# Kernel tuning notes

Measured on AMD Instinct MI355X. Metric: run time of the kernel, lower is better.

## Reference

```python
import jax, jax.numpy as jnp
import numpy as np


def conv(x, w, b=None, stride=1, pad=0):
    out = jax.lax.conv_general_dilated(x, w, (stride, stride), [(pad, pad), (pad, pad)],
                                       dimension_numbers=('NCHW', 'OIHW', 'NCHW'))
    if b is not None:
        out = out + b[None, :, None, None]
    return out


def fsm(x, att_w, conv_w):
    # FeatureSelectionModule: global-avg-pool -> 1x1 conv -> sigmoid gate, residual, 1x1 proj
    gap = jnp.mean(x, axis=(2, 3), keepdims=True)
    atten = jax.nn.sigmoid(conv(gap, att_w))
    return conv(x + x * atten, conv_w)


def mdcn(x, offset, mask, weight, bias, pad=1, G=8):
    # Modulated deformable conv v2: stride 1, dilation 1, conv groups 1, G deformable groups.
    N, C, H, W = x.shape
    Co, Ci, kh, kw = weight.shape
    K = kh * kw
    Cg = C // G
    off = offset.reshape(N, G, 2, K, H, W)          # per-group (y, x) offsets per kernel tap
    msk = mask.reshape(N, G, 1, K, H, W)
    ky, kx = jnp.meshgrid(jnp.arange(kh), jnp.arange(kw), indexing='ij')
    py = (jnp.arange(H, dtype=x.dtype)[None, None, None, :, None] - pad) + ky.reshape(1, 1, K, 1, 1) + off[:, :, 0]
    px = (jnp.arange(W, dtype=x.dtype)[None, None, None, None, :] - pad) + kx.reshape(1, 1, K, 1, 1) + off[:, :, 1]
    y0 = jnp.floor(py)
    x0 = jnp.floor(px)
    wy1 = py - y0
    wy0 = 1.0 - wy1
    wx1 = px - x0
    wx0 = 1.0 - wx1
    xg = x.reshape(N, G, Cg, H * W)

    def gather(iy, ix):
        valid = (iy >= 0) & (iy <= H - 1) & (ix >= 0) & (ix <= W - 1)
        idx = (jnp.clip(iy, 0, H - 1) * W + jnp.clip(ix, 0, W - 1)).astype(jnp.int32)
        v = jnp.take_along_axis(xg, idx.reshape(N, G, 1, K * H * W), axis=3)
        return v.reshape(N, G, Cg, K, H, W) * valid[:, :, None].astype(x.dtype)

    val = ((wy0 * wx0)[:, :, None] * gather(y0, x0)
         + (wy0 * wx1)[:, :, None] * gather(y0, x0 + 1)
         + (wy1 * wx0)[:, :, None] * gather(y0 + 1, x0)
         + (wy1 * wx1)[:, :, None] * gather(y0 + 1, x0 + 1))
    val = val * msk                                   # [N,G,Cg,K,H,W]
    out = jnp.einsum('ngckhw,ogck->nohw', val, weight.reshape(Co, G, Cg, K))
    return out + bias[None, :, None, None]


def align(feat_l, feat_s, att_w, fsm_w, off_w, om_w, om_b, dcn_w, dcn_b):
    # FeatureAlign_V2
    N, Cs, H, W = feat_s.shape[0], feat_s.shape[1], feat_l.shape[2], feat_l.shape[3]
    feat_up = jax.image.resize(feat_s, (N, Cs, H, W), 'bilinear')  # align_corners=False
    feat_arm = fsm(feat_l, att_w, fsm_w)
    off_feat = conv(jnp.concatenate([feat_arm, feat_up * 2.0], axis=1), off_w)
    om = conv(off_feat, om_w, om_b, pad=1)            # conv_offset_mask: 3*G*K channels
    o1, o2, mk = jnp.split(om, 3, axis=1)
    offset = jnp.concatenate([o1, o2], axis=1)
    mask = jax.nn.sigmoid(mk)
    feat_align = jax.nn.relu(mdcn(feat_up, offset, mask, dcn_w, dcn_b))
    return feat_align + feat_arm


def setup_inputs() -> dict:
    key = jax.random.key(0)
    ks = iter(jax.random.split(key, 64))

    def w(shape):
        fan_in = shape[1] * shape[2] * shape[3]
        return jax.random.normal(next(ks), shape, jnp.float32) / np.float32(np.sqrt(fan_in))

    def b(n):
        return jnp.zeros((n,), jnp.float32)

    d = {}
    d['c2'] = jax.random.normal(next(ks), (1, 256, 128, 128), jnp.float32)
    d['c3'] = jax.random.normal(next(ks), (1, 512, 64, 64), jnp.float32)
    d['c4'] = jax.random.normal(next(ks), (1, 1024, 32, 32), jnp.float32)
    d['c5'] = jax.random.normal(next(ks), (1, 2048, 16, 16), jnp.float32)
    OC = 256
    OM = 8 * 3 * 9  # deformable_groups * (2 offsets + 1 mask) * k*k = 216
    for tag, in_nc in (('16', 1024), ('8', 512), ('4', 256)):
        d['att_w' + tag] = w((in_nc, in_nc, 1, 1))
        d['fsm_w' + tag] = w((OC, in_nc, 1, 1))
        d['off_w' + tag] = w((OC, 2 * OC, 1, 1))
        d['om_w' + tag] = w((OM, OC, 3, 3))
        d['om_b' + tag] = b(OM)
        d['dcn_w' + tag] = w((OC, OC, 3, 3))
        d['dcn_b' + tag] = b(OC)
        d['out_w' + tag] = w((OC, OC, 3, 3))
        d['out_b' + tag] = b(OC)
    d['lat_w'] = w((OC, 2048, 1, 1))
    d['lat_b'] = b(OC)
    return d


def reference(c2, c3, c4, c5,
              att_w16, fsm_w16, off_w16, om_w16, om_b16, dcn_w16, dcn_b16, out_w16, out_b16,
              att_w8, fsm_w8, off_w8, om_w8, om_b8, dcn_w8, dcn_b8, out_w8, out_b8,
              att_w4, fsm_w4, off_w4, om_w4, om_b4, dcn_w4, dcn_b4, out_w4, out_b4,
              lat_w, lat_b):
    # top-down pass, coarsest first (matches FAN.forward with reversed inputs)
    p5 = conv(c5, lat_w, lat_b)
    f16 = align(c4, p5, att_w16, fsm_w16, off_w16, om_w16, om_b16, dcn_w16, dcn_b16)
    p4 = conv(f16, out_w16, out_b16, pad=1)
    f8 = align(c3, f16, att_w8, fsm_w8, off_w8, om_w8, om_b8, dcn_w8, dcn_b8)
    p3 = conv(f8, out_w8, out_b8, pad=1)
    f4 = align(c2, f8, att_w4, fsm_w4, off_w4, om_w4, om_b4, dcn_w4, dcn_b4)
    p2 = conv(f4, out_w4, out_b4, pad=1)
    return (p2, p3, p4, p5)
```

## Files before the change

kernel.cpp:

```cpp
#include <hip/hip_runtime.h>
#include <hip/hip_bf16.h>

typedef __hip_bfloat16 bf16;
typedef __attribute__((ext_vector_type(8))) short bf16x8;
typedef __attribute__((ext_vector_type(4))) float floatx4;

__device__ __forceinline__ float b2f(bf16 v) { return __bfloat162float(v); }
__device__ __forceinline__ bf16 f2b(float v) { return __float2bfloat16(v); }
__device__ __forceinline__ float us2f(unsigned short u) {
  union { unsigned int i; float f; } v; v.i = ((unsigned int)u) << 16; return v.f;
}
__device__ __forceinline__ unsigned short f2us(float f) {
  bf16 h = f2b(f); return *(unsigned short*)&h;
}

__global__ __launch_bounds__(256) void gap_kernel(const float* __restrict__ x,
                                                  float* __restrict__ gap,
                                                  int HW, float inv) {
  int c = blockIdx.x;
  const float* p = x + (size_t)c * HW;
  float s = 0.f;
  for (int i = threadIdx.x; i < HW; i += 256) s += p[i];
  __shared__ float red[256];
  red[threadIdx.x] = s;
  __syncthreads();
  for (int w = 128; w > 0; w >>= 1) {
    if (threadIdx.x < w) red[threadIdx.x] += red[threadIdx.x + w];
    __syncthreads();
  }
  if (threadIdx.x == 0) gap[c] = red[0] * inv;
}

__global__ __launch_bounds__(256) void atten_kernel(const float* __restrict__ w,
                                                    const float* __restrict__ gap,
                                                    float* __restrict__ scale, int Ci) {
  int wave = threadIdx.x >> 6, lane = threadIdx.x & 63;
  int o = blockIdx.x * 4 + wave;
  const float4* wr = (const float4*)(w + (size_t)o * Ci);
  const float4* g4 = (const float4*)gap;
  int n4 = Ci >> 2;
  float s = 0.f;
  for (int i = lane; i < n4; i += 64) {
    float4 a = wr[i], b = g4[i];
    s += a.x * b.x + a.y * b.y + a.z * b.z + a.w * b.w;
  }
#pragma unroll
  for (int off = 32; off > 0; off >>= 1) s += __shfl_down(s, off);
  if (lane == 0) scale[o] = 1.f + 1.f / (1.f + expf(-s));
}

__global__ __launch_bounds__(256) void upsample2x_nhwc_kernel(
    const bf16* __restrict__ src, bf16* __restrict__ dst, int Hs, int Ws) {
  int p = blockIdx.x;
  int c = threadIdx.x;
  int W = Ws * 2;
  int y = p / W, x = p - y * W;
  float fy = y * 0.5f - 0.25f;
  float fx = x * 0.5f - 0.25f;
  int y0 = (int)floorf(fy), x0 = (int)floorf(fx);
  float wy1 = fy - (float)y0, wx1 = fx - (float)x0;
  int y0c = min(max(y0, 0), Hs - 1);
  int y1c = min(max(y0 + 1, 0), Hs - 1);
  int x0c = min(max(x0, 0), Ws - 1);
  int x1c = min(max(x0 + 1, 0), Ws - 1);
  float v00 = b2f(src[(size_t)(y0c * Ws + x0c) * 256 + c]);
  float v01 = b2f(src[(size_t)(y0c * Ws + x1c) * 256 + c]);
  float v10 = b2f(src[(size_t)(y1c * Ws + x0c) * 256 + c]);
  float v11 = b2f(src[(size_t)(y1c * Ws + x1c) * 256 + c]);
  float v = (1.f - wy1) * ((1.f - wx1) * v00 + wx1 * v01)
          + wy1 * ((1.f - wx1) * v10 + wx1 * v11);
  dst[(size_t)p * 256 + c] = f2b(v);
}

__global__ __launch_bounds__(256) void packw1_kernel(const float* __restrict__ w,
                                                     bf16* __restrict__ BP, int K) {
  int idx = blockIdx.x * 256 + threadIdx.x;
  int j = idx & 7;
  int o = (idx >> 3) & 255;
  int kc8 = idx >> 11;
  int k = kc8 * 8 + j;
  BP[idx] = f2b(w[(size_t)o * K + k]);
}

__global__ __launch_bounds__(256) void packwd_kernel(const float* __restrict__ w,
                                                     bf16* __restrict__ BP) {
  int idx = blockIdx.x * 256 + threadIdx.x;
  int j = idx & 7;
  int o = (idx >> 3) & 255;
  int k8 = idx >> 11;
  int k = k8 * 8 + j;
  int tap = k >> 8;
  int ci = k & 255;
  BP[idx] = f2b(w[((size_t)o * 256 + ci) * 9 + tap]);
}

__global__ __launch_bounds__(256) void packw3_kernel(const float* __restrict__ w,
                                                     bf16* __restrict__ BP,
                                                     int Ci, int Co) {
  int idx = blockIdx.x * 256 + threadIdx.x;
  int total = Ci * 9 * 256;
  if (idx >= total) return;
  int j = idx & 7;
  int t1 = idx >> 3;
  int o = t1 & 255;
  int t2 = t1 >> 8;
  int q = t2 & 3;
  int t3 = t2 >> 2;
  int tap = t3 % 9;
  int c = t3 / 9;
  int ci = c * 32 + q * 8 + j;
  float v = (o < Co) ? w[((size_t)o * Ci + ci) * 9 + tap] : 0.f;
  BP[idx] = f2b(v);
}

template <bool NCHW1, typename TA1>
__global__ __launch_bounds__(256) void conv1x1_mfma_kernel(
    const TA1* __restrict__ A1, const float* __restrict__ scaleA,
    const bf16* __restrict__ A2, float scaleB,
    int Ci1, int Ci2, int HW,
    const bf16* __restrict__ BP, const float* __restrict__ bias,
    float* __restrict__ out1, bf16* __restrict__ out2, int ns2) {
  __shared__ __align__(16) bf16 sA[1024];
  int p0 = blockIdx.x * 32;
  int tid = threadIdx.x;
  int pix = tid & 31, sub = tid >> 5;
  int pix2 = tid >> 3, sub8 = tid & 7;
  int lane = tid & 63, wave = tid >> 6;
  int pg = wave & 1, cg = wave >> 1;
  int q = lane >> 4, n = lane & 15;

  floatx4 acc[4];
#pragma unroll
  for (int nt = 0; nt < 4; ++nt) acc[nt] = (floatx4)0.f;

  int nch = (Ci1 + Ci2) >> 5;
  for (int kc = 0; kc < nch; ++kc) {
    int ci0 = kc << 5;
    if (NCHW1 && ci0 < Ci1) {
#pragma unroll
      for (int it = 0; it < 4; ++it) {
        int cil = it * 8 + sub;
        float x = (float)A1[(size_t)(ci0 + cil) * HW + p0 + pix];
        if (scaleA) x *= scaleA[ci0 + cil];
        sA[((cil >> 3) * 32 + pix) * 8 + (cil & 7)] = f2b(x);
      }
    } else {
      const bf16* src; int cb; bool scl;
      if (!NCHW1 && ci0 < Ci1) {
        src = (const bf16*)(const void*)A1; cb = ci0; scl = false;
      } else {
        src = A2; cb = ci0 - Ci1; scl = true;
      }
      ushort4 raw = *(const ushort4*)&src[(size_t)(p0 + pix2) * 256 + cb + sub8 * 4];
      if (scl) {
        raw.x = f2us(us2f(raw.x) * scaleB);
        raw.y = f2us(us2f(raw.y) * scaleB);
        raw.z = f2us(us2f(raw.z) * scaleB);
        raw.w = f2us(us2f(raw.w) * scaleB);
      }
      *(ushort4*)&sA[((sub8 >> 1) * 32 + pix2) * 8 + (sub8 & 1) * 4] = raw;
    }
    __syncthreads();
    bf16x8 a = *(const bf16x8*)&sA[(q * 32 + pg * 16 + n) * 8];
    const bf16* bp = BP + ((size_t)(kc * 4 + q) * 256 + blockIdx.y * 128 + cg * 64) * 8;
#pragma unroll
    for (int nt = 0; nt < 4; ++nt) {
      bf16x8 b = *(const bf16x8*)&bp[(nt * 16 + n) * 8];
      acc[nt] = __builtin_amdgcn_mfma_f32_16x16x32_bf16(a, b, acc[nt], 0, 0, 0);
    }
    __syncthreads();
  }

  int pbase = p0 + pg * 16 + q * 4;
#pragma unroll
  for (int nt = 0; nt < 4; ++nt) {
    int o = blockIdx.y * 128 + cg * 64 + nt * 16 + n;
    float bv = bias ? bias[o] : 0.f;
#pragma unroll
    for (int r = 0; r < 4; ++r) {
      float v = acc[nt][r] + bv;
      if (out1) out1[(size_t)o * HW + pbase + r] = v;
      if (out2) out2[(size_t)(pbase + r) * ns2 + o] = f2b(v);
    }
  }
}

__global__ __launch_bounds__(256) void conv1x1_part_kernel(
    const float* __restrict__ A1, int HW,
    const bf16* __restrict__ BP, float* __restrict__ PART) {
  __shared__ __align__(16) bf16 sA[1024];
  int p0 = blockIdx.x * 32;
  int tid = threadIdx.x;
  int pix = tid & 31, sub = tid >> 5;
  int lane = tid & 63, wave = tid >> 6;
  int pg = wave & 1, cg = wave >> 1;
  int q = lane >> 4, n = lane & 15;

  floatx4 acc[4];
#pragma unroll
  for (int nt = 0; nt < 4; ++nt) acc[nt] = (floatx4)0.f;

  int kc0 = blockIdx.z * 8;
  for (int kcl = 0; kcl < 8; ++kcl) {
    int kc = kc0 + kcl;
    int ci0 = kc << 5;
#pragma unroll
    for (int it = 0; it < 4; ++it) {
      int cil = it * 8 + sub;
      sA[((cil >> 3) * 32 + pix) * 8 + (cil & 7)] =
          f2b(A1[(size_t)(ci0 + cil) * HW + p0 + pix]);
    }
    __syncthreads();
    bf16x8 a = *(const bf16x8*)&sA[(q * 32 + pg * 16 + n) * 8];
    const bf16* bp = BP + ((size_t)(kc * 4 + q) * 256 + blockIdx.y * 128 + cg * 64) * 8;
#pragma unroll
    for (int nt = 0; nt < 4; ++nt) {
      bf16x8 b = *(const bf16x8*)&bp[(nt * 16 + n) * 8];
      acc[nt] = __builtin_amdgcn_mfma_f32_16x16x32_bf16(a, b, acc[nt], 0, 0, 0);
    }
    __syncthreads();
  }

  int pbase = p0 + pg * 16 + q * 4;
#pragma unroll
  for (int nt = 0; nt < 4; ++nt) {
    int o = blockIdx.y * 128 + cg * 64 + nt * 16 + n;
#pragma unroll
    for (int r = 0; r < 4; ++r)
      PART[((size_t)blockIdx.z * 256 + o) * HW + pbase + r] = acc[nt][r];
  }
}

__global__ __launch_bounds__(256) void reduce_p5_kernel(
    const float* __restrict__ PART, const float* __restrict__ bias,
    float* __restrict__ out1, bf16* __restrict__ out2, int HW, int KS) {
  int o = blockIdx.x;
  int p = threadIdx.x;
  float s = bias[o];
  for (int z = 0; z < KS; ++z) s += PART[((size_t)z * 256 + o) * HW + p];
  out1[(size_t)o * HW + p] = s;
  out2[(size_t)p * 256 + o] = f2b(s);
}

template <int S>
__global__ __launch_bounds__(256) void conv3x3v2_kernel(
    const bf16* __restrict__ in, const bf16* __restrict__ BP,
    const float* __restrict__ bias,
    int H, int W, int Co,
    float* __restrict__ out1, bf16* __restrict__ out2, int ns2) {
  constexpr int P = 32 * S + 2;
  constexpr int TASKS = 3 * P * 8;
  constexpr int ITS = (TASKS + 255) / 256;
  __shared__ __align__(16) bf16 sA[2][4 * 3 * P * 8];
  int HW = H * W;
  int segs = W / (32 * S);
  int y = blockIdx.x / segs;
  int x0 = (blockIdx.x - y * segs) * (32 * S);
  int tid = threadIdx.x;
  int lane = tid & 63, wave = tid >> 6;
  int pg = wave & 1, cg = wave >> 1;
  int q = lane >> 4, n = lane & 15;

  int dstIdx[ITS], srcOff[ITS];
  bool act[ITS], val[ITS];
#pragma unroll
  for (int it = 0; it < ITS; ++it) {
    int tt = it * 256 + tid;
    act[it] = (tt < TASKS);
    int sub8 = tt & 7;
    int rp = tt >> 3;
    int row = rp / P;
    int pxl = rp - row * P;
    int yy = y + row - 1;
    int xg = x0 + pxl - 1;
    bool v = act[it] && ((unsigned)yy < (unsigned)H) && ((unsigned)xg < (unsigned)W);
    val[it] = v;
    srcOff[it] = v ? ((yy * W + xg) * 256 + sub8 * 4) : 0;
    dstIdx[it] = (((sub8 >> 1) * 3 + row) * P + pxl) * 8 + (sub8 & 1) * 4;
  }

  ushort4 pv[ITS];
  auto load_regs = [&](int kc) {
    int cb = kc << 5;
#pragma unroll
    for (int it = 0; it < ITS; ++it) {
      ushort4 z = {0, 0, 0, 0};
      pv[it] = val[it] ? *(const ushort4*)&in[(size_t)srcOff[it] + cb] : z;
    }
  };
  auto store_lds = [&](int buf) {
#pragma unroll
    for (int it = 0; it < ITS; ++it)
      if (act[it]) *(ushort4*)&sA[buf][dstIdx[it]] = pv[it];
  };

  floatx4 acc[S][4];
#pragma unroll
  for (int s = 0; s < S; ++s)
#pragma unroll
    for (int nt = 0; nt < 4; ++nt) acc[s][nt] = (floatx4)0.f;

  load_regs(0);
  store_lds(0);
  __syncthreads();
  load_regs(1);

  for (int kc = 0; kc < 8; ++kc) {
    const bf16* sv = &sA[kc & 1][0];
    const bf16* bpc = BP + (size_t)kc * 73728;
#pragma unroll
    for (int tap = 0; tap < 9; ++tap) {
      int ty = tap / 3, tx = tap % 3;
      bf16x8 a[S];
#pragma unroll
      for (int s = 0; s < S; ++s)
        a[s] = *(const bf16x8*)&sv[((q * 3 + ty) * P + tx + s * 32 + pg * 16 + n) * 8];
      const bf16* bp = bpc + ((size_t)(tap * 4 + q) * 256 + blockIdx.y * 128 + cg * 64) * 8;
#pragma unroll
      for (int nt = 0; nt < 4; ++nt) {
        bf16x8 b = *(const bf16x8*)&bp[(nt * 16 + n) * 8];
#pragma unroll
        for (int s = 0; s < S; ++s)
          acc[s][nt] = __builtin_amdgcn_mfma_f32_16x16x32_bf16(a[s], b, acc[s][nt], 0, 0, 0);
      }
    }
    if (kc < 7) {
      store_lds((kc + 1) & 1);
      __syncthreads();
      if (kc < 6) load_regs(kc + 2);
    }
  }

#pragma unroll
  for (int s = 0; s < S; ++s) {
    int pbase = y * W + x0 + s * 32 + pg * 16 + q * 4;
#pragma unroll
    for (int nt = 0; nt < 4; ++nt) {
      int o = blockIdx.y * 128 + cg * 64 + nt * 16 + n;
      if (o < Co) {
        float bv = bias ? bias[o] : 0.f;
#pragma unroll
        for (int r = 0; r < 4; ++r) {
          float v = acc[s][nt][r] + bv;
          if (out1) out1[(size_t)o * HW + pbase + r] = v;
          if (out2) out2[(size_t)(pbase + r) * ns2 + o] = f2b(v);
        }
      }
    }
  }
}

__global__ __launch_bounds__(512, 4) void mdcn_mfma_kernel(
    const bf16* __restrict__ UPn, const bf16* __restrict__ OM,
    const bf16* __restrict__ BP, const float* __restrict__ dcn_b,
    const bf16* __restrict__ ARM, bf16* __restrict__ F,
    int H, int W, int wshift) {
  __shared__ __align__(16) bf16 sval[2][32 * 272];
  __shared__ float4 mw[2304];
  __shared__ int mi[2304];
  int pb = blockIdx.x * 32;
  int tid = threadIdx.x;

  for (int t2 = tid; t2 < 2304; t2 += 512) {
    int px_ = t2 & 31, g = (t2 >> 5) & 7, tap = t2 >> 8;
    int ky = tap / 3, kx = tap - ky * 3;
    int p = pb + px_;
    int y = p >> wshift, x = p & (W - 1);
    const bf16* omp = OM + (size_t)p * 216;
    float dy = b2f(omp[g * 18 + tap]);
    float dx = b2f(omp[g * 18 + 9 + tap]);
    float mm = 1.f / (1.f + expf(-b2f(omp[144 + g * 9 + tap])));
    float fpy = (float)(y - 1 + ky) + dy;
    float fpx = (float)(x - 1 + kx) + dx;
    fpy = fminf(fmaxf(fpy, -1.0e4f), 1.0e4f);
    fpx = fminf(fmaxf(fpx, -1.0e4f), 1.0e4f);
    float fy0 = floorf(fpy), fx0 = floorf(fpx);
    float wy1 = fpy - fy0, wx1 = fpx - fx0;
    float wy0 = 1.f - wy1, wx0 = 1.f - wx1;
    int iy0 = (int)fy0, ix0 = (int)fx0;
    bool vy0 = (unsigned)iy0 < (unsigned)H;
    bool vy1 = (unsigned)(iy0 + 1) < (unsigned)H;
    bool vx0 = (unsigned)ix0 < (unsigned)W;
    bool vx1 = (unsigned)(ix0 + 1) < (unsigned)W;
    float w00 = (vy0 && vx0) ? mm * wy0 * wx0 : 0.f;
    float w01 = (vy0 && vx1) ? mm * wy0 * wx1 : 0.f;
    float w10 = (vy1 && vx0) ? mm * wy1 * wx0 : 0.f;
    float w11 = (vy1 && vx1) ? mm * wy1 * wx1 : 0.f;
    int iy0c = min(max(iy0, 0), H - 1);
    int iy1c = min(max(iy0 + 1, 0), H - 1);
    int ix0c = min(max(ix0, 0), W - 1);
    int ix1c = min(max(ix0 + 1, 0), W - 1);
    mw[t2] = make_float4(w00, w01, w10, w11);
    mi[t2] = (iy0c * W + ix0c) | ((ix1c - ix0c) << 20) | ((iy1c - iy0c) << 21);
  }
  __syncthreads();

  int px = tid >> 4, l2 = tid & 15;
  int lane = tid & 63, wave = tid >> 6;
  int q = lane >> 4, n = lane & 15;
  int rowb = l2 >> 2;
  int woff = px * 8 + (l2 & 3) * 2;

  floatx4 acc[2][2];
#pragma unroll
  for (int m = 0; m < 2; ++m)
#pragma unroll
    for (int nt = 0; nt < 2; ++nt) acc[m][nt] = (floatx4)0.f;

  auto gather = [&](int t) {
    bf16* sv = &sval[t & 1][0];
    int base = t * 256 + px;
#pragma unroll
    for (int g = 0; g < 8; ++g) {
      float4 wv = mw[base + g * 32];
      int mv = mi[base + g * 32];
      int idx = mv & 0x3FFFF;
      int dxs = (mv >> 20) & 1;
      int dyW = ((mv >> 21) & 1) * W;
      const bf16* up = UPn + (size_t)idx * 256 + g * 32 + l2 * 2;
      ushort2 u00 = *(const ushort2*)(up);
      ushort2 u01 = *(const ushort2*)(up + dxs * 256);
      ushort2 u10 = *(const ushort2*)(up + dyW * 256);
      ushort2 u11 = *(const ushort2*)(up + (dyW + dxs) * 256);
      float s0 = wv.x * us2f(u00.x) + wv.y * us2f(u01.x)
               + wv.z * us2f(u10.x) + wv.w * us2f(u11.x);
      float s1 = wv.x * us2f(u00.y) + wv.y * us2f(u01.y)
               + wv.z * us2f(u10.y) + wv.w * us2f(u11.y);
      ushort2 o2;
      o2.x = f2us(s0);
      o2.y = f2us(s1);
      *(ushort2*)&sv[(g * 4 + rowb) * 272 + woff] = o2;
    }
  };

  gather(0);
  for (int t = 0; t < 9; ++t) {
    __syncthreads();
    if (t < 8) gather(t + 1);
    const bf16* sv = &sval[t & 1][0];
    const bf16* bpt = BP + ((size_t)(t * 32) * 256 + wave * 32) * 8;
#pragma unroll
    for (int kc = 0; kc < 8; ++kc) {
      int R = kc * 4 + q;
      bf16x8 a0 = *(const bf16x8*)&sv[R * 272 + n * 8];
      bf16x8 a1 = *(const bf16x8*)&sv[R * 272 + (16 + n) * 8];
      const bf16* bp = bpt + (size_t)R * 2048;
      bf16x8 b0 = *(const bf16x8*)&bp[n * 8];
      bf16x8 b1 = *(const bf16x8*)&bp[(16 + n) * 8];
      acc[0][0] = __builtin_amdgcn_mfma_f32_16x16x32_bf16(a0, b0, acc[0][0], 0, 0, 0);
      acc[0][1] = __builtin_amdgcn_mfma_f32_16x16x32_bf16(a0, b1, acc[0][1], 0, 0, 0);
      acc[1][0] = __builtin_amdgcn_mfma_f32_16x16x32_bf16(a1, b0, acc[1][0], 0, 0, 0);
      acc[1][1] = __builtin_amdgcn_mfma_f32_16x16x32_bf16(a1, b1, acc[1][1], 0, 0, 0);
    }
  }

#pragma unroll
  for (int m = 0; m < 2; ++m) {
#pragma unroll
    for (int nt = 0; nt < 2; ++nt) {
      int o = wave * 32 + nt * 16 + n;
      float bv = dcn_b[o];
#pragma unroll
      for (int r = 0; r < 4; ++r) {
        int p = pb + m * 16 + q * 4 + r;
        float v = fmaxf(acc[m][nt][r] + bv, 0.f) + b2f(ARM[(size_t)p * 256 + o]);
        F[(size_t)p * 256 + o] = f2b(v);
      }
    }
  }
}

extern "C" void kernel_launch(void* const* d_in, const int* in_sizes, int n_in,
                              void* d_out, int out_size, void* d_ws, size_t ws_size,
                              hipStream_t stream) {
  const float* c2 = (const float*)d_in[0];
  const float* c3 = (const float*)d_in[1];
  const float* c4 = (const float*)d_in[2];
  const float* c5 = (const float*)d_in[3];
  const float* lat_w = (const float*)d_in[31];
  const float* lat_b = (const float*)d_in[32];
  float* out = (float*)d_out;
  (void)ws_size; (void)in_sizes; (void)n_in; (void)out_size;

  const size_t p2_off = 0;
  const size_t p3_off = 4194304;
  const size_t p4_off = p3_off + 1048576;
  const size_t p5_off = p4_off + 262144;

  char* ws = (char*)d_ws;
  bf16* UPn = (bf16*)(ws);
  bf16* ARM = (bf16*)(ws + 8388608);
  bf16* FB  = (bf16*)(ws + 16777216);
  bf16* P5N = (bf16*)(ws + 25165824);
  bf16* BPB = (bf16*)(ws + 25296896);
  float* GAP = (float*)(ws + 26476544);
  float* SC  = (float*)(ws + 26484736);
  bf16* OM = (bf16*)(out + p2_off);
  float* PART = (float*)ws;

  packw1_kernel<<<2048, 256, 0, stream>>>(lat_w, BPB, 2048);
  conv1x1_part_kernel<<<dim3(8, 2, 8), 256, 0, stream>>>(c5, 256, BPB, PART);
  reduce_p5_kernel<<<256, 256, 0, stream>>>(PART, lat_b, out + p5_off, P5N, 256, 8);

  struct Lv {
    const float* featl; int Ci; int H; int W; int wshift;
    float* pdst; int wbase;
  };
  Lv levels[3] = {
      {c4, 1024, 32, 32, 5, out + p4_off, 4},
      {c3, 512, 64, 64, 6, out + p3_off, 13},
      {c2, 256, 128, 128, 7, out + p2_off, 22},
  };

  for (int li = 0; li < 3; ++li) {
    const Lv& L = levels[li];
    const float* att_w = (const float*)d_in[L.wbase + 0];
    const float* fsm_w = (const float*)d_in[L.wbase + 1];
    const float* off_w = (const float*)d_in[L.wbase + 2];
    const float* om_w  = (const float*)d_in[L.wbase + 3];
    const float* om_b  = (const float*)d_in[L.wbase + 4];
    const float* dcn_w = (const float*)d_in[L.wbase + 5];
    const float* dcn_b = (const float*)d_in[L.wbase + 6];
    const float* out_w = (const float*)d_in[L.wbase + 7];
    const float* out_b = (const float*)d_in[L.wbase + 8];
    int HW = L.H * L.W;

    upsample2x_nhwc_kernel<<<HW, 256, 0, stream>>>(
        (li == 0) ? P5N : FB, UPn, L.H / 2, L.W / 2);
    gap_kernel<<<L.Ci, 256, 0, stream>>>(L.featl, GAP, HW, 1.f / (float)HW);
    atten_kernel<<<L.Ci / 4, 256, 0, stream>>>(att_w, GAP, SC, L.Ci);
    packw1_kernel<<<L.Ci, 256, 0, stream>>>(fsm_w, BPB, L.Ci);
    conv1x1_mfma_kernel<true, float><<<dim3(HW / 32, 2), 256, 0, stream>>>(
        L.featl, SC, nullptr, 0.f, L.Ci, 0, HW, BPB, nullptr,
        nullptr, ARM, 256);
    packw1_kernel<<<512, 256, 0, stream>>>(off_w, BPB, 512);
    conv1x1_mfma_kernel<false, bf16><<<dim3(HW / 32, 2), 256, 0, stream>>>(
        ARM, nullptr, UPn, 2.f, 256, 256, HW, BPB, nullptr,
        nullptr, FB, 256);
    packw3_kernel<<<2304, 256, 0, stream>>>(om_w, BPB, 256, 216);
    if (li == 2)
      conv3x3v2_kernel<2><<<dim3(HW / 64, 2), 256, 0, stream>>>(
          FB, BPB, om_b, L.H, L.W, 216, nullptr, OM, 216);
    else
      conv3x3v2_kernel<1><<<dim3(HW / 32, 2), 256, 0, stream>>>(
          FB, BPB, om_b, L.H, L.W, 216, nullptr, OM, 216);
    packwd_kernel<<<2304, 256, 0, stream>>>(dcn_w, BPB);
    mdcn_mfma_kernel<<<HW / 32, 512, 0, stream>>>(
        UPn, OM, BPB, dcn_b, ARM, FB, L.H, L.W, L.wshift);
    packw3_kernel<<<2304, 256, 0, stream>>>(out_w, BPB, 256, 256);
    if (li == 2)
      conv3x3v2_kernel<2><<<dim3(HW / 64, 2), 256, 0, stream>>>(
          FB, BPB, out_b, L.H, L.W, 256, L.pdst, nullptr, 256);
    else
      conv3x3v2_kernel<1><<<dim3(HW / 32, 2), 256, 0, stream>>>(
          FB, BPB, out_b, L.H, L.W, 256, L.pdst, nullptr, 256);
  }
}
```

Measured before the change: 733.3 us.

## Restructure deformable conv kernel: 64-pixel tiles, per-thread sampling, vectorized gathers

The MDCN kernel now covers 64 pixels per block instead of 32, so each weight fragment loaded from global memory feeds four M-tiles of MFMA instead of two. The shared-memory precompute table of bilinear weights and indices is gone. Each thread computes its own sample coordinates per tap inside the gather, and loads 8-channel vectors (four 16-byte loads per corner) instead of 2-channel pairs. This cuts weight traffic and shared-memory bookkeeping per pixel, but adds recomputation of offsets, higher register pressure (occupancy hint lowered to 2) and half as many blocks.

```diff
diff --git a/kernel.cpp b/kernel.cpp
--- a/kernel.cpp
+++ b/kernel.cpp
@@ -4,6 +4,7 @@
 typedef __hip_bfloat16 bf16;
 typedef __attribute__((ext_vector_type(8))) short bf16x8;
 typedef __attribute__((ext_vector_type(4))) float floatx4;
+typedef __attribute__((ext_vector_type(8))) unsigned short ushort8v;
 
 __device__ __forceinline__ float b2f(bf16 v) { return __bfloat162float(v); }
 __device__ __forceinline__ bf16 f2b(float v) { return __float2bfloat16(v); }
@@ -350,26 +351,35 @@
   }
 }
 
-__global__ __launch_bounds__(512, 4) void mdcn_mfma_kernel(
+__global__ __launch_bounds__(512, 2) void mdcn_mfma_kernel(
     const bf16* __restrict__ UPn, const bf16* __restrict__ OM,
     const bf16* __restrict__ BP, const float* __restrict__ dcn_b,
     const bf16* __restrict__ ARM, bf16* __restrict__ F,
     int H, int W, int wshift) {
-  __shared__ __align__(16) bf16 sval[2][32 * 272];
-  __shared__ float4 mw[2304];
-  __shared__ int mi[2304];
-  int pb = blockIdx.x * 32;
+  __shared__ __align__(16) bf16 sval[2][32 * 520];
+  int pb = blockIdx.x * 64;
   int tid = threadIdx.x;
-
-  for (int t2 = tid; t2 < 2304; t2 += 512) {
-    int px_ = t2 & 31, g = (t2 >> 5) & 7, tap = t2 >> 8;
-    int ky = tap / 3, kx = tap - ky * 3;
-    int p = pb + px_;
-    int y = p >> wshift, x = p & (W - 1);
-    const bf16* omp = OM + (size_t)p * 216;
-    float dy = b2f(omp[g * 18 + tap]);
-    float dx = b2f(omp[g * 18 + 9 + tap]);
-    float mm = 1.f / (1.f + expf(-b2f(omp[144 + g * 9 + tap])));
+  int g = tid >> 6;
+  int px = tid & 63;
+  int p = pb + px;
+  int y = p >> wshift, x = p & (W - 1);
+  const bf16* omp = OM + (size_t)p * 216 + g * 18;
+  const bf16* omm = OM + (size_t)p * 216 + 144 + g * 9;
+  int lane = tid & 63, wave = tid >> 6;
+  int q = lane >> 4, n = lane & 15;
+
+  floatx4 acc[4][2];
+#pragma unroll
+  for (int m = 0; m < 4; ++m)
+#pragma unroll
+    for (int nt = 0; nt < 2; ++nt) acc[m][nt] = (floatx4)0.f;
+
+  auto gather = [&](int t) {
+    bf16* sv = &sval[t & 1][0];
+    int ky = t / 3, kx = t - ky * 3;
+    float dy = b2f(omp[t]);
+    float dx = b2f(omp[9 + t]);
+    float mm = 1.f / (1.f + expf(-b2f(omm[t])));
     float fpy = (float)(y - 1 + ky) + dy;
     float fpx = (float)(x - 1 + kx) + dx;
     fpy = fminf(fmaxf(fpy, -1.0e4f), 1.0e4f);
@@ -390,46 +400,24 @@
     int iy1c = min(max(iy0 + 1, 0), H - 1);
     int ix0c = min(max(ix0, 0), W - 1);
     int ix1c = min(max(ix0 + 1, 0), W - 1);
-    mw[t2] = make_float4(w00, w01, w10, w11);
-    mi[t2] = (iy0c * W + ix0c) | ((ix1c - ix0c) << 20) | ((iy1c - iy0c) << 21);
-  }
-  __syncthreads();
-
-  int px = tid >> 4, l2 = tid & 15;
-  int lane = tid & 63, wave = tid >> 6;
-  int q = lane >> 4, n = lane & 15;
-  int rowb = l2 >> 2;
-  int woff = px * 8 + (l2 & 3) * 2;
-
-  floatx4 acc[2][2];
-#pragma unroll
-  for (int m = 0; m < 2; ++m)
-#pragma unroll
-    for (int nt = 0; nt < 2; ++nt) acc[m][nt] = (floatx4)0.f;
-
-  auto gather = [&](int t) {
-    bf16* sv = &sval[t & 1][0];
-    int base = t * 256 + px;
-#pragma unroll
-    for (int g = 0; g < 8; ++g) {
-      float4 wv = mw[base + g * 32];
-      int mv = mi[base + g * 32];
-      int idx = mv & 0x3FFFF;
-      int dxs = (mv >> 20) & 1;
-      int dyW = ((mv >> 21) & 1) * W;
-      const bf16* up = UPn + (size_t)idx * 256 + g * 32 + l2 * 2;
-      ushort2 u00 = *(const ushort2*)(up);
-      ushort2 u01 = *(const ushort2*)(up + dxs * 256);
-      ushort2 u10 = *(const ushort2*)(up + dyW * 256);
-      ushort2 u11 = *(const ushort2*)(up + (dyW + dxs) * 256);
-      float s0 = wv.x * us2f(u00.x) + wv.y * us2f(u01.x)
-               + wv.z * us2f(u10.x) + wv.w * us2f(u11.x);
-      float s1 = wv.x * us2f(u00.y) + wv.y * us2f(u01.y)
-               + wv.z * us2f(u10.y) + wv.w * us2f(u11.y);
-      ushort2 o2;
-      o2.x = f2us(s0);
-      o2.y = f2us(s1);
-      *(ushort2*)&sv[(g * 4 + rowb) * 272 + woff] = o2;
+    int dxs = (ix1c - ix0c) * 256;
+    int dyW = (iy1c - iy0c) * W * 256;
+    const bf16* up = UPn + (size_t)(iy0c * W + ix0c) * 256 + g * 32;
+#pragma unroll
+    for (int cc = 0; cc < 4; ++cc) {
+      const bf16* b0 = up + cc * 8;
+      ushort8v u00 = *(const ushort8v*)(b0);
+      ushort8v u01 = *(const ushort8v*)(b0 + dxs);
+      ushort8v u10 = *(const ushort8v*)(b0 + dyW);
+      ushort8v u11 = *(const ushort8v*)(b0 + dyW + dxs);
+      ushort8v o;
+#pragma unroll
+      for (int j = 0; j < 8; ++j) {
+        float s = w00 * us2f(u00[j]) + w01 * us2f(u01[j])
+                + w10 * us2f(u10[j]) + w11 * us2f(u11[j]);
+        o[j] = f2us(s);
+      }
+      *(ushort8v*)&sv[(g * 4 + cc) * 520 + px * 8] = o;
     }
   };
 
@@ -442,29 +430,29 @@
 #pragma unroll
     for (int kc = 0; kc < 8; ++kc) {
       int R = kc * 4 + q;
-      bf16x8 a0 = *(const bf16x8*)&sv[R * 272 + n * 8];
-      bf16x8 a1 = *(const bf16x8*)&sv[R * 272 + (16 + n) * 8];
       const bf16* bp = bpt + (size_t)R * 2048;
       bf16x8 b0 = *(const bf16x8*)&bp[n * 8];
       bf16x8 b1 = *(const bf16x8*)&bp[(16 + n) * 8];
-      acc[0][0] = __builtin_amdgcn_mfma_f32_16x16x32_bf16(a0, b0, acc[0][0], 0, 0, 0);
-      acc[0][1] = __builtin_amdgcn_mfma_f32_16x16x32_bf16(a0, b1, acc[0][1], 0, 0, 0);
-      acc[1][0] = __builtin_amdgcn_mfma_f32_16x16x32_bf16(a1, b0, acc[1][0], 0, 0, 0);
-      acc[1][1] = __builtin_amdgcn_mfma_f32_16x16x32_bf16(a1, b1, acc[1][1], 0, 0, 0);
-    }
-  }
-
-#pragma unroll
-  for (int m = 0; m < 2; ++m) {
+#pragma unroll
+      for (int m = 0; m < 4; ++m) {
+        bf16x8 a = *(const bf16x8*)&sv[R * 520 + (m * 16 + n) * 8];
+        acc[m][0] = __builtin_amdgcn_mfma_f32_16x16x32_bf16(a, b0, acc[m][0], 0, 0, 0);
+        acc[m][1] = __builtin_amdgcn_mfma_f32_16x16x32_bf16(a, b1, acc[m][1], 0, 0, 0);
+      }
+    }
+  }
+
+#pragma unroll
+  for (int m = 0; m < 4; ++m) {
 #pragma unroll
     for (int nt = 0; nt < 2; ++nt) {
       int o = wave * 32 + nt * 16 + n;
       float bv = dcn_b[o];
 #pragma unroll
       for (int r = 0; r < 4; ++r) {
-        int p = pb + m * 16 + q * 4 + r;
-        float v = fmaxf(acc[m][nt][r] + bv, 0.f) + b2f(ARM[(size_t)p * 256 + o]);
-        F[(size_t)p * 256 + o] = f2b(v);
+        int pp = pb + m * 16 + q * 4 + r;
+        float v = fmaxf(acc[m][nt][r] + bv, 0.f) + b2f(ARM[(size_t)pp * 256 + o]);
+        F[(size_t)pp * 256 + o] = f2b(v);
       }
     }
   }
@@ -545,7 +533,7 @@
       conv3x3v2_kernel<1><<<dim3(HW / 32, 2), 256, 0, stream>>>(
           FB, BPB, om_b, L.H, L.W, 216, nullptr, OM, 216);
     packwd_kernel<<<2304, 256, 0, stream>>>(dcn_w, BPB);
-    mdcn_mfma_kernel<<<HW / 32, 512, 0, stream>>>(
+    mdcn_mfma_kernel<<<HW / 64, 512, 0, stream>>>(
         UPn, OM, BPB, dcn_b, ARM, FB, L.H, L.W, L.wshift);
     packw3_kernel<<<2304, 256, 0, stream>>>(out_w, BPB, 256, 256);
     if (li == 2)
```

After: 832.8 us. 1.14x slower.
